# Performance work log

Measured on AMD Instinct MI355X. Metric: run time of the kernel, lower is better.

Reference implementation:

```python
import jax, jax.numpy as jnp
import numpy as np

B, T, C, H = 8, 1024, 1024, 16
D = C // H
EPS = 1e-5

def _ln(x, g, b):
    mu = jnp.mean(x, axis=-1, keepdims=True)
    var = jnp.var(x, axis=-1, keepdims=True)
    return (x - mu) * jax.lax.rsqrt(var + EPS) * g + b

def _build_mask(cond_mask, cond_len, token_len):
    # Vectorized form of the per-batch Python-loop mask in the torch module.
    counts = jnp.sum(cond_mask, axis=-1)            # [B] number of valid cond tokens
    rows = jnp.arange(T)
    cols = jnp.arange(T)
    # all rows may attend to the first counts[i] (cond) columns
    m_cond = cols[None, None, :] < counts[:, None, None]          # [B,1,T]
    m_cond = jnp.broadcast_to(m_cond, (B, T, T))
    # block-causal tiled pattern on rows/cols >= cond_len:
    # value = (col - cond_len) % token_len <= (row - cond_len) % token_len
    pattern = ((cols[None, :] - cond_len) % token_len) <= ((rows[:, None] - cond_len) % token_len)
    m_block = (rows[:, None] >= cond_len) & (cols[None, :] >= cond_len) & pattern  # [T,T]
    # cols >= cond_len: overwritten by block pattern (rows < cond_len stay 0 there)
    mask = jnp.where(cols[None, None, :] < cond_len, m_cond, m_block[None, :, :])
    return mask[:, None, :, :]                      # [B,1,T,T] bool

def _attn(x, Wq, bq, Wk, bk, Wv, bv, Wp, bp, cond_mask, cond_len, token_len):
    q = (x @ Wq + bq).reshape(B, T, H, D).transpose(0, 2, 1, 3)  # [B,H,T,D]
    k = (x @ Wk + bk).reshape(B, T, H, D).transpose(0, 2, 1, 3)
    v = (x @ Wv + bv).reshape(B, T, H, D).transpose(0, 2, 1, 3)
    att = jnp.einsum('bhqd,bhkd->bhqk', q, k) * (1.0 / np.sqrt(D))
    mask = _build_mask(cond_mask, cond_len, token_len)
    att = jnp.where(mask, att, -jnp.inf)
    att = jax.nn.softmax(att, axis=-1)
    y = jnp.einsum('bhqk,bhkd->bhqd', att, v)
    y = y.transpose(0, 2, 1, 3).reshape(B, T, C)
    return y @ Wp + bp

def setup_inputs() -> dict:
    key = jax.random.key(0)
    ks = jax.random.split(key, 16)
    cond_len, token_len = 256, 768
    s = 1.0 / np.sqrt(C)
    counts = jax.random.randint(ks[0], (B,), 1, cond_len + 1)
    cond_mask = (jnp.arange(T)[None, :] < counts[:, None]).astype(jnp.int32)
    return {
        'x': jax.random.normal(ks[1], (B, T, C), jnp.float32),
        'ln1_g': jnp.ones((C,), jnp.float32), 'ln1_b': jnp.zeros((C,), jnp.float32),
        'Wq': jax.random.normal(ks[2], (C, C), jnp.float32) * s, 'bq': jnp.zeros((C,), jnp.float32),
        'Wk': jax.random.normal(ks[3], (C, C), jnp.float32) * s, 'bk': jnp.zeros((C,), jnp.float32),
        'Wv': jax.random.normal(ks[4], (C, C), jnp.float32) * s, 'bv': jnp.zeros((C,), jnp.float32),
        'Wp': jax.random.normal(ks[5], (C, C), jnp.float32) * s, 'bp': jnp.zeros((C,), jnp.float32),
        'ln2_g': jnp.ones((C,), jnp.float32), 'ln2_b': jnp.zeros((C,), jnp.float32),
        'W1': jax.random.normal(ks[6], (C, 4 * C), jnp.float32) * s, 'b1': jnp.zeros((4 * C,), jnp.float32),
        'W2': jax.random.normal(ks[7], (4 * C, C), jnp.float32) * (0.5 * s), 'b2': jnp.zeros((C,), jnp.float32),
        'cond_mask': cond_mask,
        'cond_len': cond_len,
        'token_len': token_len,
    }

def reference(x, ln1_g, ln1_b, Wq, bq, Wk, bk, Wv, bv, Wp, bp, ln2_g, ln2_b, W1, b1, W2, b2, cond_mask, cond_len, token_len):
    x = x + _attn(_ln(x, ln1_g, ln1_b), Wq, bq, Wk, bk, Wv, bv, Wp, bp, cond_mask, cond_len, token_len)
    h = _ln(x, ln2_g, ln2_b)
    x = x + (jax.nn.gelu(h @ W1 + b1, approximate=False) @ W2 + b2)
    return x
```

## Files before the change

kernel.cpp:

```cpp
#include <hip/hip_runtime.h>
#include <hip/hip_bf16.h>
#include <cstdint>
#include <cstddef>

typedef __attribute__((ext_vector_type(8))) short short8;
typedef __attribute__((ext_vector_type(4))) float f32x4;
typedef __attribute__((ext_vector_type(4))) unsigned short us4;

#define MFMA_BF16(a, b, c) __builtin_amdgcn_mfma_f32_16x16x32_bf16((a), (b), (c), 0, 0, 0)
#define VMCNT(n) asm volatile("s_waitcnt vmcnt(" #n ")" ::: "memory")

__device__ __forceinline__ unsigned short f2bf(float f) {
  unsigned int u = __float_as_uint(f);
  u += 0x7FFFu + ((u >> 16) & 1u);
  return (unsigned short)(u >> 16);
}

typedef const void __attribute__((address_space(1)))* as1_cvp;
typedef void __attribute__((address_space(3)))* as3_vp;
__device__ __forceinline__ void gll16(const short* g, short* l) {
#if defined(__HIP_DEVICE_COMPILE__)
  __builtin_amdgcn_global_load_lds((as1_cvp)g, (as3_vp)l, 16, 0, 0);
#else
  (void)g; (void)l;
#endif
}

__global__ void count_kernel(const int* __restrict__ cm, int* __restrict__ counts) {
  __shared__ int sd[256];
  const int b = blockIdx.x, t = threadIdx.x;
  int s = 0;
  for (int i = t; i < 1024; i += 256) s += cm[b * 1024 + i];
  sd[t] = s; __syncthreads();
  for (int k = 128; k > 0; k >>= 1) { if (t < k) sd[t] += sd[t + k]; __syncthreads(); }
  if (t == 0) counts[b] = sd[0];
}

__global__ void pack_bias_kernel(const float* __restrict__ bq, const float* __restrict__ bk,
                                 const float* __restrict__ bv, float* __restrict__ dst) {
  int i = blockIdx.x * 256 + threadIdx.x;
  dst[i] = (i < 1024) ? bq[i] : (i < 2048 ? bk[i - 1024] : bv[i - 2048]);
}

__global__ void transpose_kernel(const float* __restrict__ src, unsigned short* __restrict__ dst,
                                 int R, int C) {
  __shared__ float tile[32][33];
  const int c0 = blockIdx.x * 32, r0 = blockIdx.y * 32;
  const int tx = threadIdx.x, ty = threadIdx.y;
  #pragma unroll
  for (int i = ty; i < 32; i += 8)
    tile[i][tx] = src[(size_t)(r0 + i) * C + (c0 + tx)];
  __syncthreads();
  #pragma unroll
  for (int i = ty; i < 32; i += 8)
    dst[(size_t)(c0 + i) * R + (r0 + tx)] = f2bf(tile[tx][i]);
}

__global__ void vtrans_kernel(const short* __restrict__ qkv, short* __restrict__ vtr) {
  __shared__ short tile[32][33];
  const int bh = blockIdx.z;
  const int t0 = blockIdx.x * 32, d0 = blockIdx.y * 32;
  const int b = bh >> 4, h = bh & 15;
  const int tx = threadIdx.x, ty = threadIdx.y;
  const short* src = qkv + (size_t)b * 1024 * 3072 + 2048 + h * 64;
  #pragma unroll
  for (int i = ty; i < 32; i += 8)
    tile[i][tx] = src[(size_t)(t0 + i) * 3072 + d0 + tx];
  __syncthreads();
  short* dst = vtr + (size_t)bh * 65536;
  #pragma unroll
  for (int i = ty; i < 32; i += 8)
    dst[(d0 + i) * 1024 + t0 + tx] = tile[tx][i];
}

__global__ __launch_bounds__(256) void ln_kernel(const float* __restrict__ in,
                                                 const float* __restrict__ gw,
                                                 const float* __restrict__ bw,
                                                 unsigned short* __restrict__ out) {
  const int row = blockIdx.x, t = threadIdx.x;
  const float4 v = ((const float4*)(in + (size_t)row * 1024))[t];
  float s = v.x + v.y + v.z + v.w;
  float ss = v.x * v.x + v.y * v.y + v.z * v.z + v.w * v.w;
  #pragma unroll
  for (int o = 32; o >= 1; o >>= 1) { s += __shfl_down(s, o, 64); ss += __shfl_down(ss, o, 64); }
  __shared__ float red[8];
  if ((t & 63) == 0) { red[t >> 6] = s; red[4 + (t >> 6)] = ss; }
  __syncthreads();
  const float S  = red[0] + red[1] + red[2] + red[3];
  const float SS = red[4] + red[5] + red[6] + red[7];
  const float mu = S * (1.0f / 1024.0f);
  const float var = SS * (1.0f / 1024.0f) - mu * mu;
  const float rs = rsqrtf(var + 1e-5f);
  const int c = t * 4;
  const float4 g4 = ((const float4*)gw)[t];
  const float4 b4 = ((const float4*)bw)[t];
  us4 o4;
  o4[0] = f2bf((v.x - mu) * rs * g4.x + b4.x);
  o4[1] = f2bf((v.y - mu) * rs * g4.y + b4.y);
  o4[2] = f2bf((v.z - mu) * rs * g4.z + b4.z);
  o4[3] = f2bf((v.w - mu) * rs * g4.w + b4.w);
  *(us4*)(out + (size_t)row * 1024 + c) = o4;
}

template <int EPI>
__global__ __launch_bounds__(256) void gemm_bt_kernel(
    const short* __restrict__ A, const short* __restrict__ BT,
    const float* __restrict__ bias, int N, int K,
    unsigned short* __restrict__ outb, float* __restrict__ outf,
    const float* __restrict__ res) {
  __shared__ alignas(16) short As[4096];
  __shared__ alignas(16) short Bs[4096];
  const int t = threadIdx.x;
  const int l = t & 63, w = t >> 6;
  const int lq = l & 15, g = l >> 4;
  const int wr = w >> 1, wc = w & 1;
  const int bm = blockIdx.x * 128, bn = blockIdx.y * 128;

  const f32x4 z4 = {0.f, 0.f, 0.f, 0.f};
  f32x4 acc[4][4];
  #pragma unroll
  for (int i = 0; i < 4; i++)
    #pragma unroll
    for (int j = 0; j < 4; j++) acc[i][j] = z4;

  const short* ga = A  + (size_t)(bm + (t >> 2)) * K + (t & 3) * 8;
  const short* gb = BT + (size_t)(bn + (t >> 2)) * K + (t & 3) * 8;
  short* lA = As + w * 512;
  short* lB = Bs + w * 512;

  for (int k0 = 0; k0 < K; k0 += 32) {
    gll16(ga + k0,                  lA);
    gll16(ga + k0 + (size_t)64 * K, lA + 2048);
    gll16(gb + k0,                  lB);
    gll16(gb + k0 + (size_t)64 * K, lB + 2048);
    __syncthreads();
    short8 af[4], bfr[4];
    #pragma unroll
    for (int mi = 0; mi < 4; mi++)
      af[mi] = *(const short8*)(As + (wr * 64 + mi * 16 + lq) * 32 + 8 * g);
    #pragma unroll
    for (int ni = 0; ni < 4; ni++)
      bfr[ni] = *(const short8*)(Bs + (wc * 64 + ni * 16 + lq) * 32 + 8 * g);
    #pragma unroll
    for (int mi = 0; mi < 4; mi++)
      #pragma unroll
      for (int ni = 0; ni < 4; ni++)
        acc[mi][ni] = MFMA_BF16(af[mi], bfr[ni], acc[mi][ni]);
    __syncthreads();
  }

  #pragma unroll
  for (int mi = 0; mi < 4; mi++) {
    #pragma unroll
    for (int ni = 0; ni < 4; ni++) {
      const int col = bn + wc * 64 + ni * 16 + lq;
      const float bv = bias[col];
      #pragma unroll
      for (int r = 0; r < 4; r++) {
        const int row = bm + wr * 64 + mi * 16 + 4 * g + r;
        float v = acc[mi][ni][r] + bv;
        const size_t idx = (size_t)row * N + col;
        if (EPI == 1) v = 0.5f * v * (1.0f + erff(v * 0.70710678118654752440f));
        if (EPI == 2) outf[idx] = v + res[idx];
        else          outb[idx] = f2bf(v);
      }
    }
  }
}

template <int EPI>
__global__ __launch_bounds__(512, 2) void gemm256_kernel(
    const short* __restrict__ A, const short* __restrict__ BT,
    const float* __restrict__ bias, int N, int K,
    unsigned short* __restrict__ outb) {
  __shared__ alignas(16) short lds[65536];
  const int t = threadIdx.x;
  const int l = t & 63, w = t >> 6;
  const int lq = l & 15, g = l >> 4;
  const int wr = w >> 2, wc = w & 3;
  const int bm = blockIdx.x * 256, bn = blockIdx.y * 256;
  const int NT = K >> 6;

  const int csw = ((t & 7) ^ ((t >> 3) & 7)) * 8;
  const int sA = t >> 3;
  const int sB = ((t >> 8) & 1) * 64 + ((t >> 3) & 31);

  const f32x4 z4 = {0.f, 0.f, 0.f, 0.f};
  f32x4 acc[8][4];
  #pragma unroll
  for (int i = 0; i < 8; i++)
    #pragma unroll
    for (int j = 0; j < 4; j++) acc[i][j] = z4;

  auto stageA = [&](int buf, int h, int k0) {
    const short* src = A + (size_t)(bm + h * 64 + sA) * K + k0 + csw;
    short* dst = lds + buf * 32768 + h * 8192 + t * 8;
    gll16(src, dst);
    gll16(src + (size_t)128 * K, dst + 4096);
  };
  auto stageB = [&](int buf, int h, int k0) {
    const short* src = BT + (size_t)(bn + h * 32 + sB) * K + k0 + csw;
    short* dst = lds + buf * 32768 + 16384 + h * 8192 + t * 8;
    gll16(src, dst);
    gll16(src + (size_t)128 * K, dst + 4096);
  };
  auto rdA = [&](int buf, int mh, int mi2, int kk) {
    const int ra = wr * 64 + mi2 * 16 + lq;
    const int unit = (kk * 4 + g) ^ (ra & 7);
    return *(const short8*)(lds + buf * 32768 + mh * 8192 + ra * 64 + unit * 8);
  };
  auto rdB = [&](int buf, int nh, int ni2, int kk) {
    const int rb = wc * 32 + ni2 * 16 + lq;
    const int unit = (kk * 4 + g) ^ (rb & 7);
    return *(const short8*)(lds + buf * 32768 + 16384 + nh * 8192 + rb * 64 + unit * 8);
  };

  stageA(0, 0, 0);  stageB(0, 0, 0);
  stageA(0, 1, 0);  stageB(0, 1, 0);
  stageA(1, 0, 64); stageB(1, 0, 64);
  VMCNT(8);
  __builtin_amdgcn_s_barrier();

  short8 a[4][2], b0[2][2], b1[2][2];
  for (int v = 0; v < NT; ++v) {
    const int cur = v & 1, nxt = cur ^ 1;
    #pragma unroll
    for (int mi2 = 0; mi2 < 4; ++mi2)
      #pragma unroll
      for (int kk = 0; kk < 2; ++kk) a[mi2][kk] = rdA(cur, 0, mi2, kk);
    #pragma unroll
    for (int ni2 = 0; ni2 < 2; ++ni2)
      #pragma unroll
      for (int kk = 0; kk < 2; ++kk) b0[ni2][kk] = rdB(cur, 0, ni2, kk);
    if (v + 1 < NT) stageA(nxt, 1, (v + 1) * 64);
    if (v + 1 < NT) { VMCNT(6); } else { VMCNT(0); }
    __builtin_amdgcn_s_barrier();
    __builtin_amdgcn_s_setprio(1);
    #pragma unroll
    for (int mi2 = 0; mi2 < 4; ++mi2)
      #pragma unroll
      for (int ni2 = 0; ni2 < 2; ++ni2)
        #pragma unroll
        for (int kk = 0; kk < 2; ++kk)
          acc[mi2][ni2] = MFMA_BF16(a[mi2][kk], b0[ni2][kk], acc[mi2][ni2]);
    __builtin_amdgcn_s_setprio(0);
    __builtin_amdgcn_s_barrier();
    #pragma unroll
    for (int ni2 = 0; ni2 < 2; ++ni2)
      #pragma unroll
      for (int kk = 0; kk < 2; ++kk) b1[ni2][kk] = rdB(cur, 1, ni2, kk);
    if (v + 1 < NT) stageB(nxt, 1, (v + 1) * 64);
    __builtin_amdgcn_s_barrier();
    __builtin_amdgcn_s_setprio(1);
    #pragma unroll
    for (int mi2 = 0; mi2 < 4; ++mi2)
      #pragma unroll
      for (int ni2 = 0; ni2 < 2; ++ni2)
        #pragma unroll
        for (int kk = 0; kk < 2; ++kk)
          acc[mi2][2 + ni2] = MFMA_BF16(a[mi2][kk], b1[ni2][kk], acc[mi2][2 + ni2]);
    __builtin_amdgcn_s_setprio(0);
    __builtin_amdgcn_s_barrier();
    #pragma unroll
    for (int mi2 = 0; mi2 < 4; ++mi2)
      #pragma unroll
      for (int kk = 0; kk < 2; ++kk) a[mi2][kk] = rdA(cur, 1, mi2, kk);
    if (v + 2 < NT) stageA(cur, 0, (v + 2) * 64);
    __builtin_amdgcn_s_barrier();
    __builtin_amdgcn_s_setprio(1);
    #pragma unroll
    for (int mi2 = 0; mi2 < 4; ++mi2)
      #pragma unroll
      for (int ni2 = 0; ni2 < 2; ++ni2)
        #pragma unroll
        for (int kk = 0; kk < 2; ++kk)
          acc[4 + mi2][ni2] = MFMA_BF16(a[mi2][kk], b0[ni2][kk], acc[4 + mi2][ni2]);
    __builtin_amdgcn_s_setprio(0);
    __builtin_amdgcn_s_barrier();
    if (v + 2 < NT) stageB(cur, 0, (v + 2) * 64);
    if (v + 1 < NT) {
      if (v + 2 < NT) { VMCNT(8); } else { VMCNT(4); }
    }
    __builtin_amdgcn_s_barrier();
    __builtin_amdgcn_s_setprio(1);
    #pragma unroll
    for (int mi2 = 0; mi2 < 4; ++mi2)
      #pragma unroll
      for (int ni2 = 0; ni2 < 2; ++ni2)
        #pragma unroll
        for (int kk = 0; kk < 2; ++kk)
          acc[4 + mi2][2 + ni2] = MFMA_BF16(a[mi2][kk], b1[ni2][kk], acc[4 + mi2][2 + ni2]);
    __builtin_amdgcn_s_setprio(0);
    __builtin_amdgcn_s_barrier();
  }

  unsigned short* eb = (unsigned short*)lds;
  #pragma unroll
  for (int mi = 0; mi < 8; ++mi) {
    #pragma unroll
    for (int ni = 0; ni < 4; ++ni) {
      const int col = wc * 64 + (ni >> 1) * 32 + (ni & 1) * 16 + lq;
      const float bv = bias[bn + col];
      #pragma unroll
      for (int r = 0; r < 4; ++r) {
        const int row = wr * 128 + (mi >> 2) * 64 + (mi & 3) * 16 + 4 * g + r;
        float vv = acc[mi][ni][r] + bv;
        if (EPI == 1) vv = 0.5f * vv * (1.0f + erff(vv * 0.70710678118654752440f));
        eb[row * 256 + col] = f2bf(vv);
      }
    }
  }
  __syncthreads();
  #pragma unroll
  for (int it = 0; it < 16; ++it) {
    const int unit = it * 512 + t;
    const int row = unit >> 5, c8 = unit & 31;
    const short8 vv = *(const short8*)(lds + unit * 8);
    *(short8*)((short*)outb + (size_t)(bm + row) * N + bn + c8 * 8) = vv;
  }
}

__global__ __launch_bounds__(64) void attn_kernel(
    const short* __restrict__ qkv, const short* __restrict__ vtr,
    unsigned short* __restrict__ y, const int* __restrict__ counts) {
  const int blk = blockIdx.x;
  const int slot = blk >> 3;
  const int p = slot & 31;
  const int bh = ((slot >> 5) << 3) | (blk & 7);
  const int b = bh >> 4, h = bh & 15;
  const int l = threadIdx.x & 63;
  const int lq = l & 15, g = l >> 4;
  const int qb0 = p * 16, qb1 = (63 - p) * 16;
  const int count = counts[b];

  const short* base  = qkv + (size_t)b * 1024 * 3072 + h * 64;
  const short* vbase = vtr + (size_t)bh * 65536;

  short8 qf[2][2];
  {
    const short* qr0 = base + (size_t)(qb0 + lq) * 3072 + 8 * g;
    const short* qr1 = base + (size_t)(qb1 + lq) * 3072 + 8 * g;
    qf[0][0] = *(const short8*)qr0; qf[0][1] = *(const short8*)(qr0 + 32);
    qf[1][0] = *(const short8*)qr1; qf[1][1] = *(const short8*)(qr1 + 32);
  }

  const f32x4 z4 = {0.f, 0.f, 0.f, 0.f};
  f32x4 oacc[2][4];
  #pragma unroll
  for (int grp = 0; grp < 2; ++grp)
    #pragma unroll
    for (int dc = 0; dc < 4; ++dc) oacc[grp][dc] = z4;
  float mrun[2] = {-1e30f, -1e30f};
  float lrun[2] = {0.f, 0.f};
  const int permrow = 8 * (lq >> 2) + (lq & 3);
  const float SC = 0.125f * 1.44269504088896f;

  const int ncond = min((count + 31) >> 5, 8);
  const int ncausal = (qb1 + 16 - 256 + 31) >> 5;
  const int nt = ncond + ncausal;
  auto kv_of = [&](int i) { return i < ncond ? i * 32 : 256 + (i - ncond) * 32; };

  auto loadt = [&](int kv0, short8 (&kr)[4], short8 (&vr)[4]) {
    const short* ka = base + (size_t)(kv0 + permrow) * 3072 + 1024 + 8 * g;
    kr[0] = *(const short8*)ka;
    kr[1] = *(const short8*)(ka + 32);
    kr[2] = *(const short8*)(ka + 4 * 3072);
    kr[3] = *(const short8*)(ka + 4 * 3072 + 32);
    #pragma unroll
    for (int dc = 0; dc < 4; ++dc)
      vr[dc] = *(const short8*)(vbase + (16 * dc + lq) * 1024 + kv0 + 8 * g);
  };

  auto compute = [&](int i, const short8 (&kr)[4], const short8 (&vr)[4]) {
    const int kv0 = kv_of(i);
    const bool isCond = (i < ncond);
    #pragma unroll
    for (int grp = 0; grp < 2; ++grp) {
      const int qb = grp ? qb1 : qb0;
      if (!isCond && kv0 >= qb + 16) continue;
      const bool needMask = isCond ? (kv0 + 32 > count) : (kv0 + 31 > qb);
      f32x4 sA = z4, sB = z4;
      __builtin_amdgcn_s_setprio(1);
      sA = MFMA_BF16(kr[0], qf[grp][0], sA);
      sA = MFMA_BF16(kr[1], qf[grp][1], sA);
      sB = MFMA_BF16(kr[2], qf[grp][0], sB);
      sB = MFMA_BF16(kr[3], qf[grp][1], sB);
      __builtin_amdgcn_s_setprio(0);
      const int q = qb + lq;
      float mx = -1e30f;
      if (needMask) {
        #pragma unroll
        for (int r = 0; r < 4; ++r) {
          const int colA = kv0 + 8 * g + r, colB = colA + 4;
          const bool okA = isCond ? (colA < count) : (colA <= q);
          const bool okB = isCond ? (colB < count) : (colB <= q);
          const float vA = okA ? sA[r] * SC : -1e30f;
          const float vB = okB ? sB[r] * SC : -1e30f;
          sA[r] = vA; sB[r] = vB;
          mx = fmaxf(fmaxf(vA, vB), mx);
        }
      } else {
        #pragma unroll
        for (int r = 0; r < 4; ++r) {
          const float vA = sA[r] * SC, vB = sB[r] * SC;
          sA[r] = vA; sB[r] = vB;
          mx = fmaxf(fmaxf(vA, vB), mx);
        }
      }
      mx = fmaxf(mx, __shfl_xor(mx, 16, 64));
      mx = fmaxf(mx, __shfl_xor(mx, 32, 64));
      float m = mrun[grp];
      if (!__all(mx <= m + 8.0f)) {
        const float mn = fmaxf(m, mx);
        const float sf = exp2f(m - mn);
        lrun[grp] *= sf;
        #pragma unroll
        for (int dc = 0; dc < 4; ++dc)
          #pragma unroll
          for (int r = 0; r < 4; ++r) oacc[grp][dc][r] *= sf;
        mrun[grp] = mn; m = mn;
      }
      float ps = 0.f;
      #pragma unroll
      for (int r = 0; r < 4; ++r) {
        const float aa = exp2f(sA[r] - m);
        const float c2 = exp2f(sB[r] - m);
        sA[r] = aa; sB[r] = c2; ps += aa + c2;
      }
      ps += __shfl_xor(ps, 16, 64);
      ps += __shfl_xor(ps, 32, 64);
      lrun[grp] += ps;
      union { short8 s8; __hip_bfloat162 h2[4]; } pu;
      pu.h2[0] = __float22bfloat162_rn(float2{sA[0], sA[1]});
      pu.h2[1] = __float22bfloat162_rn(float2{sA[2], sA[3]});
      pu.h2[2] = __float22bfloat162_rn(float2{sB[0], sB[1]});
      pu.h2[3] = __float22bfloat162_rn(float2{sB[2], sB[3]});
      __builtin_amdgcn_s_setprio(1);
      #pragma unroll
      for (int dc = 0; dc < 4; ++dc)
        oacc[grp][dc] = MFMA_BF16(vr[dc], pu.s8, oacc[grp][dc]);
      __builtin_amdgcn_s_setprio(0);
    }
  };

  short8 kb0[4], vb0[4], kb1[4], vb1[4];
  loadt(kv_of(0), kb0, vb0);
  for (int i = 0; i < nt; i += 2) {
    if (i + 1 < nt) loadt(kv_of(i + 1), kb1, vb1);
    compute(i, kb0, vb0);
    if (i + 1 >= nt) break;
    if (i + 2 < nt) loadt(kv_of(i + 2), kb0, vb0);
    compute(i + 1, kb1, vb1);
  }

  #pragma unroll
  for (int grp = 0; grp < 2; ++grp) {
    const int qb = grp ? qb1 : qb0;
    const float inv = 1.0f / lrun[grp];
    unsigned short* yr = y + (size_t)(b * 1024 + qb + lq) * 1024 + h * 64;
    #pragma unroll
    for (int dc = 0; dc < 4; ++dc)
      #pragma unroll
      for (int r = 0; r < 4; ++r)
        yr[16 * dc + 4 * g + r] = f2bf(oacc[grp][dc][r] * inv);
  }
}

extern "C" void kernel_launch(void* const* d_in, const int* in_sizes, int n_in,
                              void* d_out, int out_size, void* d_ws, size_t ws_size,
                              hipStream_t stream) {
  (void)in_sizes; (void)n_in; (void)out_size; (void)ws_size;
  const float* x     = (const float*)d_in[0];
  const float* ln1_g = (const float*)d_in[1];
  const float* ln1_b = (const float*)d_in[2];
  const float* Wq    = (const float*)d_in[3];
  const float* bq    = (const float*)d_in[4];
  const float* Wk    = (const float*)d_in[5];
  const float* bk    = (const float*)d_in[6];
  const float* Wv    = (const float*)d_in[7];
  const float* bv    = (const float*)d_in[8];
  const float* Wp    = (const float*)d_in[9];
  const float* bp    = (const float*)d_in[10];
  const float* ln2_g = (const float*)d_in[11];
  const float* ln2_b = (const float*)d_in[12];
  const float* W1    = (const float*)d_in[13];
  const float* b1    = (const float*)d_in[14];
  const float* W2    = (const float*)d_in[15];
  const float* b2    = (const float*)d_in[16];
  const int* cond_mask = (const int*)d_in[17];

  char* ws = (char*)d_ws;
  const size_t MB = 1u << 20;
  short* xn    = (short*)(ws + 0);
  short* vtr   = (short*)(ws + 0);
  short* qkv   = (short*)(ws + 16 * MB);
  short* act   = (short*)(ws + 0);
  unsigned short* yb = (unsigned short*)(ws + 64 * MB);
  float* x1    = (float*)(ws + 80 * MB);
  short* hb    = (short*)(ws + 112 * MB);
  short* wqkvT = (short*)(ws + 128 * MB);
  short* wpT   = (short*)(ws + 134 * MB);
  short* w1T   = (short*)(ws + 136 * MB);
  short* w2T   = (short*)(ws + 144 * MB);
  float* bqkv  = (float*)(ws + 152 * MB);
  int* counts  = (int*)(ws + 152 * MB + 16384);

  const dim3 tb(32, 8);
  count_kernel<<<8, 256, 0, stream>>>(cond_mask, counts);
  pack_bias_kernel<<<12, 256, 0, stream>>>(bq, bk, bv, bqkv);
  transpose_kernel<<<dim3(32, 32), tb, 0, stream>>>(Wq, (unsigned short*)wqkvT, 1024, 1024);
  transpose_kernel<<<dim3(32, 32), tb, 0, stream>>>(Wk, (unsigned short*)(wqkvT + 1024 * 1024), 1024, 1024);
  transpose_kernel<<<dim3(32, 32), tb, 0, stream>>>(Wv, (unsigned short*)(wqkvT + 2 * 1024 * 1024), 1024, 1024);
  transpose_kernel<<<dim3(32, 32), tb, 0, stream>>>(Wp, (unsigned short*)wpT, 1024, 1024);
  transpose_kernel<<<dim3(128, 32), tb, 0, stream>>>(W1, (unsigned short*)w1T, 1024, 4096);
  transpose_kernel<<<dim3(32, 128), tb, 0, stream>>>(W2, (unsigned short*)w2T, 4096, 1024);
  ln_kernel<<<8192, 256, 0, stream>>>(x, ln1_g, ln1_b, (unsigned short*)xn);

  gemm256_kernel<0><<<dim3(32, 12), 512, 0, stream>>>(xn, wqkvT, bqkv, 3072, 1024,
                                                      (unsigned short*)qkv);
  vtrans_kernel<<<dim3(32, 2, 128), tb, 0, stream>>>(qkv, vtr);
  attn_kernel<<<4096, 64, 0, stream>>>(qkv, vtr, yb, counts);
  gemm_bt_kernel<2><<<dim3(64, 8), 256, 0, stream>>>((const short*)yb, wpT, bp, 1024, 1024,
                                                     nullptr, x1, x);
  ln_kernel<<<8192, 256, 0, stream>>>(x1, ln2_g, ln2_b, (unsigned short*)hb);
  gemm256_kernel<1><<<dim3(32, 16), 512, 0, stream>>>(hb, w1T, b1, 4096, 1024,
                                                      (unsigned short*)act);
  gemm_bt_kernel<2><<<dim3(64, 8), 256, 0, stream>>>(act, w2T, b2, 1024, 4096,
                                                     nullptr, (float*)d_out, x1);
}
```

Before: 468.4 us.

## Route projection GEMMs through the 256-tile pipelined kernel and remap blocks across XCDs

Removes the simple 128x128 single-buffered GEMM and runs the attention output projection and the MLP down-projection on the pipelined 256x256 kernel, through a new fp32 residual-add epilogue. It also replaces the 2D grid with a 1D grid whose block index is remapped so consecutive tiles are grouped per XCD (blockIdx & 7), aiming for better L2 locality. The Wp and W2 GEMMs now launch only 128 blocks on a device with many more CUs, so under-occupancy is a risk that may cancel the per-tile efficiency gain.

```diff
diff --git a/kernel.cpp b/kernel.cpp
--- a/kernel.cpp
+++ b/kernel.cpp
@@ -103,82 +103,19 @@
 }
 
 template <int EPI>
-__global__ __launch_bounds__(256) void gemm_bt_kernel(
+__global__ __launch_bounds__(512, 2) void gemm256_kernel(
     const short* __restrict__ A, const short* __restrict__ BT,
-    const float* __restrict__ bias, int N, int K,
+    const float* __restrict__ bias, int N, int K, int gm,
     unsigned short* __restrict__ outb, float* __restrict__ outf,
     const float* __restrict__ res) {
-  __shared__ alignas(16) short As[4096];
-  __shared__ alignas(16) short Bs[4096];
-  const int t = threadIdx.x;
-  const int l = t & 63, w = t >> 6;
-  const int lq = l & 15, g = l >> 4;
-  const int wr = w >> 1, wc = w & 1;
-  const int bm = blockIdx.x * 128, bn = blockIdx.y * 128;
-
-  const f32x4 z4 = {0.f, 0.f, 0.f, 0.f};
-  f32x4 acc[4][4];
-  #pragma unroll
-  for (int i = 0; i < 4; i++)
-    #pragma unroll
-    for (int j = 0; j < 4; j++) acc[i][j] = z4;
-
-  const short* ga = A  + (size_t)(bm + (t >> 2)) * K + (t & 3) * 8;
-  const short* gb = BT + (size_t)(bn + (t >> 2)) * K + (t & 3) * 8;
-  short* lA = As + w * 512;
-  short* lB = Bs + w * 512;
-
-  for (int k0 = 0; k0 < K; k0 += 32) {
-    gll16(ga + k0,                  lA);
-    gll16(ga + k0 + (size_t)64 * K, lA + 2048);
-    gll16(gb + k0,                  lB);
-    gll16(gb + k0 + (size_t)64 * K, lB + 2048);
-    __syncthreads();
-    short8 af[4], bfr[4];
-    #pragma unroll
-    for (int mi = 0; mi < 4; mi++)
-      af[mi] = *(const short8*)(As + (wr * 64 + mi * 16 + lq) * 32 + 8 * g);
-    #pragma unroll
-    for (int ni = 0; ni < 4; ni++)
-      bfr[ni] = *(const short8*)(Bs + (wc * 64 + ni * 16 + lq) * 32 + 8 * g);
-    #pragma unroll
-    for (int mi = 0; mi < 4; mi++)
-      #pragma unroll
-      for (int ni = 0; ni < 4; ni++)
-        acc[mi][ni] = MFMA_BF16(af[mi], bfr[ni], acc[mi][ni]);
-    __syncthreads();
-  }
-
-  #pragma unroll
-  for (int mi = 0; mi < 4; mi++) {
-    #pragma unroll
-    for (int ni = 0; ni < 4; ni++) {
-      const int col = bn + wc * 64 + ni * 16 + lq;
-      const float bv = bias[col];
-      #pragma unroll
-      for (int r = 0; r < 4; r++) {
-        const int row = bm + wr * 64 + mi * 16 + 4 * g + r;
-        float v = acc[mi][ni][r] + bv;
-        const size_t idx = (size_t)row * N + col;
-        if (EPI == 1) v = 0.5f * v * (1.0f + erff(v * 0.70710678118654752440f));
-        if (EPI == 2) outf[idx] = v + res[idx];
-        else          outb[idx] = f2bf(v);
-      }
-    }
-  }
-}
-
-template <int EPI>
-__global__ __launch_bounds__(512, 2) void gemm256_kernel(
-    const short* __restrict__ A, const short* __restrict__ BT,
-    const float* __restrict__ bias, int N, int K,
-    unsigned short* __restrict__ outb) {
   __shared__ alignas(16) short lds[65536];
   const int t = threadIdx.x;
   const int l = t & 63, w = t >> 6;
   const int lq = l & 15, g = l >> 4;
   const int wr = w >> 2, wc = w & 3;
-  const int bm = blockIdx.x * 256, bn = blockIdx.y * 256;
+  const int cpx = (int)gridDim.x >> 3;
+  const int wid = ((int)blockIdx.x & 7) * cpx + ((int)blockIdx.x >> 3);
+  const int bm = (wid % gm) * 256, bn = (wid / gm) * 256;
   const int NT = K >> 6;
 
   const int csw = ((t & 7) ^ ((t >> 3) & 7)) * 8;
@@ -292,6 +229,24 @@
           acc[4 + mi2][2 + ni2] = MFMA_BF16(a[mi2][kk], b1[ni2][kk], acc[4 + mi2][2 + ni2]);
     __builtin_amdgcn_s_setprio(0);
     __builtin_amdgcn_s_barrier();
+  }
+
+  if (EPI == 2) {
+    #pragma unroll
+    for (int mi = 0; mi < 8; ++mi) {
+      #pragma unroll
+      for (int ni = 0; ni < 4; ++ni) {
+        const int col = bn + wc * 64 + (ni >> 1) * 32 + (ni & 1) * 16 + lq;
+        const float bv = bias[col];
+        #pragma unroll
+        for (int r = 0; r < 4; ++r) {
+          const int row = bm + wr * 128 + (mi >> 2) * 64 + (mi & 3) * 16 + 4 * g + r;
+          const size_t idx = (size_t)row * N + col;
+          outf[idx] = acc[mi][ni][r] + bv + res[idx];
+        }
+      }
+    }
+    return;
   }
 
   unsigned short* eb = (unsigned short*)lds;
@@ -516,15 +471,15 @@
   transpose_kernel<<<dim3(32, 128), tb, 0, stream>>>(W2, (unsigned short*)w2T, 4096, 1024);
   ln_kernel<<<8192, 256, 0, stream>>>(x, ln1_g, ln1_b, (unsigned short*)xn);
 
-  gemm256_kernel<0><<<dim3(32, 12), 512, 0, stream>>>(xn, wqkvT, bqkv, 3072, 1024,
-                                                      (unsigned short*)qkv);
+  gemm256_kernel<0><<<384, 512, 0, stream>>>(xn, wqkvT, bqkv, 3072, 1024, 32,
+                                             (unsigned short*)qkv, nullptr, nullptr);
   vtrans_kernel<<<dim3(32, 2, 128), tb, 0, stream>>>(qkv, vtr);
   attn_kernel<<<4096, 64, 0, stream>>>(qkv, vtr, yb, counts);
-  gemm_bt_kernel<2><<<dim3(64, 8), 256, 0, stream>>>((const short*)yb, wpT, bp, 1024, 1024,
-                                                     nullptr, x1, x);
+  gemm256_kernel<2><<<128, 512, 0, stream>>>((const short*)yb, wpT, bp, 1024, 1024, 32,
+                                             nullptr, x1, x);
   ln_kernel<<<8192, 256, 0, stream>>>(x1, ln2_g, ln2_b, (unsigned short*)hb);
-  gemm256_kernel<1><<<dim3(32, 16), 512, 0, stream>>>(hb, w1T, b1, 4096, 1024,
-                                                      (unsigned short*)act);
-  gemm_bt_kernel<2><<<dim3(64, 8), 256, 0, stream>>>(act, w2T, b2, 1024, 4096,
-                                                     nullptr, (float*)d_out, x1);
-}
+  gemm256_kernel<1><<<512, 512, 0, stream>>>(hb, w1T, b1, 4096, 1024, 32,
+                                             (unsigned short*)act, nullptr, nullptr);
+  gemm256_kernel<2><<<128, 512, 0, stream>>>(act, w2T, b2, 1024, 4096, 32,
+                                             nullptr, (float*)d_out, x1);
+}
```

New measurement: 490.6 us. 1.05x slower.
